# Performance work log

Hardware: AMD Instinct MI355X
Metric: run time of the kernel (lower is better)

## Reference

```python
import jax, jax.numpy as jnp
import numpy as np

N, D, C, E = 100000, 128, 16, 1000000
NUM_LAYERS, ALPHA = 5, 0.5
EPS_COS, EPS_LN = 1e-8, 1e-5


def setup_inputs() -> dict:
    key = jax.random.key(0)
    ks = jax.random.split(key, 10)
    inp = {
        'features': jax.random.normal(ks[0], (N, D), jnp.float32),
        'init_logits': jax.random.uniform(ks[1], (N, C), jnp.float32),
        'W': jax.random.normal(ks[2], (D, D), jnp.float32) * (1.0 / np.sqrt(D)),
        'b': jnp.zeros((D,), jnp.float32),
        'ln_gamma': jnp.ones((D,), jnp.float32),
        'ln_beta': jnp.zeros((D,), jnp.float32),
        'ew_connect': jnp.ones((1,), jnp.float32),
        'ew_decorate': jnp.ones((1,), jnp.float32),
        'ew_next': jnp.ones((1,), jnp.float32),
    }
    names = ['src_connect', 'dst_connect', 'src_decorate', 'dst_decorate', 'src_next', 'dst_next']
    for i, nm in enumerate(names):
        inp[nm] = jax.random.randint(ks[4 + (i % 6)] if False else jax.random.fold_in(ks[3], i), (E,), 0, N, jnp.int32)
    return inp


def _label_prop(features, init_logits, W, b, ln_gamma, ln_beta, ews, edges):
    # feature_transform: Linear -> LayerNorm -> ReLU (Dropout is identity in eval)
    h = features @ W.T + b
    mu = jnp.mean(h, axis=-1, keepdims=True)
    var = jnp.mean(jnp.square(h - mu), axis=-1, keepdims=True)
    h = (h - mu) * jax.lax.rsqrt(var + EPS_LN) * ln_gamma + ln_beta
    h = jax.nn.relu(h)
    # per-node L2-normalized features for cosine similarity (eps-clamped like F.cosine_similarity)
    nrm = jnp.maximum(jnp.linalg.norm(h, axis=-1), EPS_COS)
    hn = h / nrm[:, None]
    # per-edge scalar weights are fixed across layers: sigmoid(ew) * cos(src, dst)
    edge_w = []
    for ew, (src, dst) in zip(ews, edges):
        sim = jnp.sum(hn[src] * hn[dst], axis=-1)  # [E]
        edge_w.append(jax.nn.sigmoid(ew[0]) * sim)
    n_nodes = init_logits.shape[0]
    cur = init_logits
    for _ in range(NUM_LAYERS):
        next_logits = jnp.zeros_like(cur)
        total_w = jnp.zeros((n_nodes,), cur.dtype)
        for w, (src, dst) in zip(edge_w, edges):
            next_logits = next_logits.at[src].add(w[:, None] * cur[dst])
            total_w = total_w.at[src].add(w)
        pos = total_w > 0
        denom = jnp.where(pos, total_w, 1.0)[:, None]
        next_logits = jnp.where(pos[:, None], next_logits / denom, next_logits)
        cur = ALPHA * next_logits + (1.0 - ALPHA) * init_logits
    return cur


def reference(features, init_logits, W, b, ln_gamma, ln_beta, ew_connect, ew_decorate, ew_next,
              src_connect, dst_connect, src_decorate, dst_decorate, src_next, dst_next):
    ews = [ew_connect, ew_decorate, ew_next]
    edges = [(src_connect, dst_connect), (src_decorate, dst_decorate), (src_next, dst_next)]
    return _label_prop(features, init_logits, W, b, ln_gamma, ln_beta, ews, edges)
```

## Files before the change

### kernel.cpp

```cpp
#include <hip/hip_runtime.h>
#include <hip/hip_fp8.h>
#include <math.h>

#define DD 128
#define CC 16
#define ALPHA_ 0.5f
#define EPS_LN 1e-5f
#define EPS_COS 1e-8f

typedef _Float16 h4 __attribute__((ext_vector_type(4)));
typedef _Float16 h8 __attribute__((ext_vector_type(8)));
typedef _Float16 f16x8 __attribute__((ext_vector_type(8)));
typedef float f32x4 __attribute__((ext_vector_type(4)));
typedef long lx2 __attribute__((ext_vector_type(2)));

__device__ __forceinline__ unsigned pk_fp8x4(float v0, float v1, float v2, float v3) {
#if __has_builtin(__builtin_amdgcn_cvt_pk_fp8_f32)
    int u = 0;
    u = __builtin_amdgcn_cvt_pk_fp8_f32(v0, v1, u, false);
    u = __builtin_amdgcn_cvt_pk_fp8_f32(v2, v3, u, true);
    return (unsigned)u;
#else
    __hip_fp8_e4m3 a(v0), b(v1), c(v2), d(v3);
    return (unsigned)a.__x | ((unsigned)b.__x << 8)
         | ((unsigned)c.__x << 16) | ((unsigned)d.__x << 24);
#endif
}

__global__ __launch_bounds__(256, 2) void ft_mfma_kernel(
    const float* __restrict__ feat, const float* __restrict__ W,
    const float* __restrict__ bias, const float* __restrict__ gamma,
    const float* __restrict__ beta, unsigned* __restrict__ hn8, int N)
{
    const int lane = threadIdx.x & 63;
    const int c16  = lane & 15;
    const int g    = lane >> 4;
    const int wv   = (blockIdx.x * (int)blockDim.x + (int)threadIdx.x) >> 6;
    const int nwv  = ((int)gridDim.x * (int)blockDim.x) >> 6;

    f16x8 wf[8][4];
#pragma unroll
    for (int jt = 0; jt < 8; ++jt) {
        const float* wr = W + (size_t)(jt * 16 + c16) * 128 + g * 8;
#pragma unroll
        for (int s = 0; s < 4; ++s) {
            float4 lo = *(const float4*)(wr + s * 32);
            float4 hi = *(const float4*)(wr + s * 32 + 4);
            f16x8 f;
            f[0] = (_Float16)lo.x; f[1] = (_Float16)lo.y;
            f[2] = (_Float16)lo.z; f[3] = (_Float16)lo.w;
            f[4] = (_Float16)hi.x; f[5] = (_Float16)hi.y;
            f[6] = (_Float16)hi.z; f[7] = (_Float16)hi.w;
            wf[jt][s] = f;
        }
    }

    const int ntiles = (N + 15) >> 4;
    for (int t = wv; t < ntiles; t += nwv) {
        const int i = (t << 4) + c16;
        const float* fr = feat + (size_t)min(i, N - 1) * 128 + g * 8;
        f16x8 bf[4];
#pragma unroll
        for (int s = 0; s < 4; ++s) {
            float4 lo = *(const float4*)(fr + s * 32);
            float4 hi = *(const float4*)(fr + s * 32 + 4);
            f16x8 f;
            f[0] = (_Float16)lo.x; f[1] = (_Float16)lo.y;
            f[2] = (_Float16)lo.z; f[3] = (_Float16)lo.w;
            f[4] = (_Float16)hi.x; f[5] = (_Float16)hi.y;
            f[6] = (_Float16)hi.z; f[7] = (_Float16)hi.w;
            bf[s] = f;
        }

        f32x4 acc[8] = {};
#pragma unroll
        for (int s = 0; s < 4; ++s)
#pragma unroll
            for (int jt = 0; jt < 8; ++jt)
                acc[jt] = __builtin_amdgcn_mfma_f32_16x16x32_f16(
                    wf[jt][s], bf[s], acc[jt], 0, 0, 0);

        float s1 = 0.f, s2 = 0.f;
#pragma unroll
        for (int jt = 0; jt < 8; ++jt) {
            float4 bb = ((const float4*)bias)[jt * 4 + g];
            float h0 = acc[jt][0] + bb.x, h1 = acc[jt][1] + bb.y;
            float h2_ = acc[jt][2] + bb.z, h3 = acc[jt][3] + bb.w;
            acc[jt][0] = h0; acc[jt][1] = h1; acc[jt][2] = h2_; acc[jt][3] = h3;
            s1 += h0 + h1 + h2_ + h3;
            s2 += h0 * h0 + h1 * h1 + h2_ * h2_ + h3 * h3;
        }
        s1 += __shfl_xor(s1, 16); s1 += __shfl_xor(s1, 32);
        s2 += __shfl_xor(s2, 16); s2 += __shfl_xor(s2, 32);
        float mu   = s1 * (1.f / 128.f);
        float var  = s2 * (1.f / 128.f) - mu * mu;
        float rstd = rsqrtf(var + EPS_LN);

        float nsq = 0.f;
#pragma unroll
        for (int jt = 0; jt < 8; ++jt) {
            float4 gg = ((const float4*)gamma)[jt * 4 + g];
            float4 be = ((const float4*)beta)[jt * 4 + g];
            float v0 = fmaxf((acc[jt][0] - mu) * rstd * gg.x + be.x, 0.f);
            float v1 = fmaxf((acc[jt][1] - mu) * rstd * gg.y + be.y, 0.f);
            float v2 = fmaxf((acc[jt][2] - mu) * rstd * gg.z + be.z, 0.f);
            float v3 = fmaxf((acc[jt][3] - mu) * rstd * gg.w + be.w, 0.f);
            acc[jt][0] = v0; acc[jt][1] = v1; acc[jt][2] = v2; acc[jt][3] = v3;
            nsq += v0 * v0 + v1 * v1 + v2 * v2 + v3 * v3;
        }
        nsq += __shfl_xor(nsq, 16); nsq += __shfl_xor(nsq, 32);
        float inv = 1.f / fmaxf(sqrtf(nsq), EPS_COS);

        if (i < N) {
#pragma unroll
            for (int jt = 0; jt < 8; ++jt) {
                hn8[(size_t)i * 32 + jt * 4 + g] =
                    pk_fp8x4(acc[jt][0] * inv, acc[jt][1] * inv,
                             acc[jt][2] * inv, acc[jt][3] * inv);
            }
        }
    }
}

__global__ void bcount_kernel(const int* __restrict__ s0, const int* __restrict__ s1,
                              const int* __restrict__ s2, int* __restrict__ gcnt,
                              int E, int NB)
{
    __shared__ int cnt[512];
    const int tid = threadIdx.x;
    for (int i = tid; i < NB; i += 256) cnt[i] = 0;
    __syncthreads();
    const int tot = 3 * E;
    const int chunk = (tot + gridDim.x - 1) / gridDim.x;
    const int lo = blockIdx.x * chunk, hi = min(lo + chunk, tot);
    for (int i = lo + tid; i < hi; i += 256) {
        int src = (i < E) ? s0[i] : (i < 2 * E) ? s1[i - E] : s2[i - 2 * E];
        atomicAdd(&cnt[src >> 8], 1);
    }
    __syncthreads();
    for (int i = tid; i < NB; i += 256)
        if (cnt[i]) atomicAdd(&gcnt[i], cnt[i]);
}

__global__ void bscan_kernel(const int* __restrict__ gcnt, int* __restrict__ bbase,
                             int* __restrict__ gcur, int NB, int totE)
{
    __shared__ int wsum[4];
    const int t = threadIdx.x;
    const int lane = t & 63;
    int a0 = (2 * t     < NB) ? gcnt[2 * t]     : 0;
    int a1 = (2 * t + 1 < NB) ? gcnt[2 * t + 1] : 0;
    int ts = a0 + a1;
    int v = ts;
#pragma unroll
    for (int m = 1; m <= 32; m <<= 1) {
        int u = __shfl_up(v, m);
        if (lane >= m) v += u;
    }
    if (lane == 63) wsum[t >> 6] = v;
    __syncthreads();
    int woff = 0;
    for (int w = 0; w < (t >> 6); ++w) woff += wsum[w];
    int excl = woff + v - ts;
    if (2 * t < NB)     { bbase[2 * t]     = excl;      gcur[2 * t]     = excl; }
    if (2 * t + 1 < NB) { bbase[2 * t + 1] = excl + a0; gcur[2 * t + 1] = excl + a0; }
    if (t == 0) bbase[NB] = totE;
}

__global__ void bpart_kernel(
    const int* __restrict__ s0, const int* __restrict__ d0,
    const int* __restrict__ s1, const int* __restrict__ d1,
    const int* __restrict__ s2, const int* __restrict__ d2,
    int* __restrict__ gcur, unsigned* __restrict__ stage, int E, int NB)
{
    __shared__ int cnt[512];
    __shared__ int rbase[512];
    const int tid = threadIdx.x;
    for (int i = tid; i < NB; i += 256) cnt[i] = 0;
    __syncthreads();
    const int tot = 3 * E;
    const int chunk = (tot + gridDim.x - 1) / gridDim.x;
    const int lo = blockIdx.x * chunk, hi = min(lo + chunk, tot);
    for (int i = lo + tid; i < hi; i += 256) {
        int src = (i < E) ? s0[i] : (i < 2 * E) ? s1[i - E] : s2[i - 2 * E];
        atomicAdd(&cnt[src >> 8], 1);
    }
    __syncthreads();
    for (int i = tid; i < NB; i += 256) {
        int c = cnt[i];
        rbase[i] = c ? atomicAdd(&gcur[i], c) : 0;
        cnt[i] = 0;
    }
    __syncthreads();
    for (int i = lo + tid; i < hi; i += 256) {
        int src, dst, cls;
        if (i < E)          { src = s0[i];         dst = d0[i];         cls = 0; }
        else if (i < 2 * E) { src = s1[i - E];     dst = d1[i - E];     cls = 1; }
        else                { src = s2[i - 2 * E]; dst = d2[i - 2 * E]; cls = 2; }
        int b = src >> 8;
        int pos = rbase[b] + atomicAdd(&cnt[b], 1);
        stage[pos] = (unsigned)dst | ((unsigned)cls << 17) | ((unsigned)(src & 255) << 19);
    }
}

__global__ void csrfin_kernel(const unsigned* __restrict__ stage,
                              const int* __restrict__ bbase,
                              int* __restrict__ row_ptr, int* __restrict__ dstc_csr,
                              int N, int totE)
{
    __shared__ int cnt[256];
    __shared__ int wsum[4];
    const int b = blockIdx.x;
    const int t = threadIdx.x;
    const int lane = t & 63;
    const int lo = b << 8;
    const int base = bbase[b];
    const int m = bbase[b + 1] - base;

    cnt[t] = 0;
    __syncthreads();
    for (int i = t; i < m; i += 256)
        atomicAdd(&cnt[(stage[base + i] >> 19) & 255], 1);
    __syncthreads();
    int c = cnt[t];
    int v = c;
#pragma unroll
    for (int mm = 1; mm <= 32; mm <<= 1) {
        int u = __shfl_up(v, mm);
        if (lane >= mm) v += u;
    }
    if (lane == 63) wsum[t >> 6] = v;
    __syncthreads();
    int woff = 0;
    for (int w = 0; w < (t >> 6); ++w) woff += wsum[w];
    int excl = woff + v - c;
    if (lo + t < N) row_ptr[lo + t] = base + excl;
    if (b == 0 && t == 0) row_ptr[N] = totE;
    __syncthreads();
    cnt[t] = base + excl;
    __syncthreads();
    for (int i = t; i < m; i += 256) {
        unsigned v2 = stage[base + i];
        int pos = atomicAdd(&cnt[(v2 >> 19) & 255], 1);
        dstc_csr[pos] = (int)(v2 & 0x1FFFF) | (int)(((v2 >> 17) & 3) << 24);
    }
}

__global__ void node_sim_kernel(const unsigned char* __restrict__ hn8,
    const int* __restrict__ row_ptr, const int* __restrict__ dstc_csr,
    const float* __restrict__ ew0, const float* __restrict__ ew1,
    const float* __restrict__ ew2, unsigned* __restrict__ wq_csr,
    float* __restrict__ scl, const _Float16* __restrict__ inith,
    _Float16* __restrict__ out1, int N)
{
    const int gtid = blockIdx.x * blockDim.x + threadIdx.x;
    const int lane = threadIdx.x & 63;
    const int c16  = lane & 15;
    const int g    = lane >> 4;
    const int wv   = gtid >> 6;
    const int nwv  = (gridDim.x * blockDim.x) >> 6;
    const float sg0 = 1.f / (1.f + expf(-ew0[0]));
    const float sg1 = 1.f / (1.f + expf(-ew1[0]));
    const float sg2 = 1.f / (1.f + expf(-ew2[0]));
    const int srcl = ((c16 >> 2) << 4) | c16;
    const int j4   = c16 & 3;

    for (int n = wv; n < N; n += nwv) {
        const int beg = row_ptr[n], end = row_ptr[n + 1];
        const int deg = end - beg;
        if (deg == 0) {
            if (lane == 0) scl[n] = ALPHA_;
            if (c16 == 0) {
                h4 ivn = *(const h4*)&inith[(size_t)n * 16 + g * 4];
                h4 st;
#pragma unroll
                for (int k = 0; k < 4; ++k)
                    st[k] = (_Float16)((1.f - ALPHA_) * (float)ivn[k]);
                *(h4*)&out1[(size_t)n * 16 + g * 4] = st;
            }
            continue;
        }

        const unsigned char* sp = hn8 + (size_t)n * 128 + g * 16;
        lx2 B0 = *(const lx2*)sp;
        lx2 B1 = *(const lx2*)(sp + 64);

        float total = 0.f;
        float p1[4] = {0.f, 0.f, 0.f, 0.f};
        const int nb = (deg + 15) >> 4;
        for (int kb = 0; kb < nb; ++kb) {
            const int ebase = beg + (kb << 4);
            const int rem = end - ebase;
            int vv = (c16 < rem) ? dstc_csr[ebase + c16] : 0;
            int dl = (c16 < rem) ? (vv & 0x1FFFF) : n;
            const unsigned char* rp = hn8 + (size_t)dl * 128 + g * 16;
            lx2 A0 = *(const lx2*)rp;
            lx2 A1 = *(const lx2*)(rp + 64);
            h4 ivd = *(const h4*)&inith[(size_t)dl * 16 + g * 4];

            f32x4 acc = {0.f, 0.f, 0.f, 0.f};
            acc = __builtin_amdgcn_mfma_f32_16x16x32_fp8_fp8(A0[0], B0[0], acc, 0, 0, 0);
            acc = __builtin_amdgcn_mfma_f32_16x16x32_fp8_fp8(A0[1], B0[1], acc, 0, 0, 0);
            acc = __builtin_amdgcn_mfma_f32_16x16x32_fp8_fp8(A1[0], B1[0], acc, 0, 0, 0);
            acc = __builtin_amdgcn_mfma_f32_16x16x32_fp8_fp8(A1[1], B1[1], acc, 0, 0, 0);

            float a01  = (j4 & 1) ? acc[1] : acc[0];
            float a23  = (j4 & 1) ? acc[3] : acc[2];
            float asel = (j4 & 2) ? a23 : a01;
            float mysim = __shfl(asel, srcl);

            int cls = (vv >> 24) & 3;
            float sgc = (cls == 0) ? sg0 : (cls == 1) ? sg1 : sg2;
            float w = sgc * mysim;
            if (c16 < rem) {
                total += w;
#pragma unroll
                for (int k = 0; k < 4; ++k) p1[k] += w * (float)ivd[k];
            }

            if (g == 0 && c16 < rem) {
                int q = (int)(w * 16000.f + ((w >= 0.f) ? 0.5f : -0.5f)) + 16384;
                q = min(max(q, 0), 32767);
                wq_csr[ebase + c16] = ((unsigned)vv & 0x1FFFFu)
                                    | ((unsigned)q << 17);
            }
        }
        total += __shfl_xor(total, 1);
        total += __shfl_xor(total, 2);
        total += __shfl_xor(total, 4);
        total += __shfl_xor(total, 8);
#pragma unroll
        for (int k = 0; k < 4; ++k) {
            p1[k] += __shfl_xor(p1[k], 1);
            p1[k] += __shfl_xor(p1[k], 2);
            p1[k] += __shfl_xor(p1[k], 4);
            p1[k] += __shfl_xor(p1[k], 8);
        }
        float s = ALPHA_ * ((total > 0.f) ? 1.f / total : 1.f);
        if (lane == 0) scl[n] = s;
        if (c16 == 0) {
            h4 ivn = *(const h4*)&inith[(size_t)n * 16 + g * 4];
            h4 st;
#pragma unroll
            for (int k = 0; k < 4; ++k)
                st[k] = (_Float16)(s * p1[k] + (1.f - ALPHA_) * (float)ivn[k]);
            *(h4*)&out1[(size_t)n * 16 + g * 4] = st;
        }
    }
}

__global__ void cvt_kernel(const float* __restrict__ init,
                           _Float16* __restrict__ outh, int M4)
{
    int i = blockIdx.x * blockDim.x + threadIdx.x;
    int stride = gridDim.x * blockDim.x;
    for (; i < M4; i += stride) {
        float4 v = ((const float4*)init)[i];
        h4 o;
        o[0] = (_Float16)v.x; o[1] = (_Float16)v.y;
        o[2] = (_Float16)v.z; o[3] = (_Float16)v.w;
        ((h4*)outh)[i] = o;
    }
}

template<bool LAST>
__global__ void prop_kernel(const int* __restrict__ row_ptr,
    const unsigned* __restrict__ wq_csr, const float* __restrict__ scl,
    const _Float16* __restrict__ cur, const _Float16* __restrict__ inith,
    float* __restrict__ out32, _Float16* __restrict__ out16, int N)
{
    const int gtid = blockIdx.x * blockDim.x + threadIdx.x;
    const int lane = threadIdx.x & 63;
    const int half = lane >> 5;
    const int l32  = lane & 31;
    const int sg   = l32 >> 2;
    const int c4   = l32 & 3;
    const int wv   = gtid >> 6;
    const int nwv  = (gridDim.x * blockDim.x) >> 6;
    const float dq = 1.f / 16000.f;
    for (int n = 2 * wv + half; n < N; n += 2 * nwv) {
        int beg = row_ptr[n], end = row_ptr[n + 1];
        float a0 = 0.f, a1 = 0.f, a2 = 0.f, a3 = 0.f;
#pragma unroll 2
        for (int e = beg + sg; e < end; e += 8) {
            unsigned u = wq_csr[e];
            int d = (int)(u & 0x1FFFFu);
            float w = (float)((int)(u >> 17) - 16384) * dq;
            h4 cv = *(const h4*)&cur[(size_t)d * 16 + c4 * 4];
            a0 += w * (float)cv[0];
            a1 += w * (float)cv[1];
            a2 += w * (float)cv[2];
            a3 += w * (float)cv[3];
        }
#pragma unroll
        for (int m = 4; m <= 16; m <<= 1) {
            a0 += __shfl_xor(a0, m);
            a1 += __shfl_xor(a1, m);
            a2 += __shfl_xor(a2, m);
            a3 += __shfl_xor(a3, m);
        }
        if (sg == 0) {
            float sc = scl[n];
            h4 iv = *(const h4*)&inith[(size_t)n * 16 + c4 * 4];
            float r0 = sc * a0 + (1.f - ALPHA_) * (float)iv[0];
            float r1 = sc * a1 + (1.f - ALPHA_) * (float)iv[1];
            float r2 = sc * a2 + (1.f - ALPHA_) * (float)iv[2];
            float r3 = sc * a3 + (1.f - ALPHA_) * (float)iv[3];
            if (LAST) {
                float4 st; st.x = r0; st.y = r1; st.z = r2; st.w = r3;
                *(float4*)&out32[(size_t)n * 16 + c4 * 4] = st;
            } else {
                h4 st;
                st[0] = (_Float16)r0; st[1] = (_Float16)r1;
                st[2] = (_Float16)r2; st[3] = (_Float16)r3;
                *(h4*)&out16[(size_t)n * 16 + c4 * 4] = st;
            }
        }
    }
}

extern "C" void kernel_launch(void* const* d_in, const int* in_sizes, int n_in,
                              void* d_out, int out_size, void* d_ws, size_t ws_size,
                              hipStream_t stream)
{
    const float* feat  = (const float*)d_in[0];
    const float* initl = (const float*)d_in[1];
    const float* W     = (const float*)d_in[2];
    const float* b     = (const float*)d_in[3];
    const float* gam   = (const float*)d_in[4];
    const float* bet   = (const float*)d_in[5];
    const float* ew0   = (const float*)d_in[6];
    const float* ew1   = (const float*)d_in[7];
    const float* ew2   = (const float*)d_in[8];
    const int* s0  = (const int*)d_in[9];
    const int* dd0 = (const int*)d_in[10];
    const int* s1  = (const int*)d_in[11];
    const int* dd1 = (const int*)d_in[12];
    const int* s2  = (const int*)d_in[13];
    const int* dd2 = (const int*)d_in[14];

    const int N = in_sizes[0] / DD;
    const int E = in_sizes[9];
    const int totE = 3 * E;
    const int NB = (N + 255) >> 8;
    float* out = (float*)d_out;

    char* ws = (char*)d_ws;
    size_t off = 0;
    auto alloc = [&](size_t bytes) -> void* {
        void* p = ws + off;
        off += (bytes + 255) & ~(size_t)255;
        return p;
    };
    unsigned*  hn8     = (unsigned*)alloc((size_t)N * DD);
    int*       gcnt    = (int*)alloc((size_t)(NB + 1) * 4);
    int*       bbase   = (int*)alloc((size_t)(NB + 1) * 4);
    int*       gcur    = (int*)alloc((size_t)(NB + 1) * 4);
    int*       row_ptr = (int*)alloc((size_t)(N + 1) * 4);
    unsigned*  stage   = (unsigned*)alloc((size_t)totE * 4);
    int*       dstc_csr= (int*)alloc((size_t)totE * 4);
    unsigned*  wq_csr  = (unsigned*)alloc((size_t)totE * 4);
    float*     scl     = (float*)alloc((size_t)N * 4);
    _Float16*  inith   = (_Float16*)alloc((size_t)N * CC * 2);
    _Float16*  curA    = (_Float16*)alloc((size_t)N * CC * 2);
    _Float16*  curB    = (_Float16*)alloc((size_t)N * CC * 2);

    ft_mfma_kernel<<<512, 256, 0, stream>>>(feat, W, b, gam, bet, hn8, N);

    hipMemsetAsync(gcnt, 0, (size_t)NB * 4, stream);
    bcount_kernel<<<1024, 256, 0, stream>>>(s0, s1, s2, gcnt, E, NB);
    bscan_kernel<<<1, 256, 0, stream>>>(gcnt, bbase, gcur, NB, totE);
    bpart_kernel<<<1024, 256, 0, stream>>>(s0, dd0, s1, dd1, s2, dd2,
                                           gcur, stage, E, NB);
    csrfin_kernel<<<NB, 256, 0, stream>>>(stage, bbase, row_ptr, dstc_csr, N, totE);

    cvt_kernel<<<256, 256, 0, stream>>>(initl, inith, N * CC / 4);

    const int wblk = (N * 64 + 255) / 256;
    node_sim_kernel<<<wblk, 256, 0, stream>>>((const unsigned char*)hn8,
                                              row_ptr, dstc_csr,
                                              ew0, ew1, ew2, wq_csr, scl,
                                              inith, curA, N);

    const int pblk = (N * 32 + 255) / 256;
    const _Float16* cs = curA;
    _Float16* bufs[2] = { curB, curA };
    for (int layer = 0; layer < 3; ++layer) {
        _Float16* dst = bufs[layer & 1];
        prop_kernel<false><<<pblk, 256, 0, stream>>>(row_ptr, wq_csr, scl,
                                                     cs, inith, nullptr, dst, N);
        cs = dst;
    }
    prop_kernel<true><<<pblk, 256, 0, stream>>>(row_ptr, wq_csr, scl,
                                                cs, inith, out, nullptr, N);
}
```

Before: 361.0 us.

## Replace bucket count+scan with fixed-capacity buckets and fuse fp16 conversion into csrfin

```diff
diff --git a/kernel.cpp b/kernel.cpp
--- a/kernel.cpp
+++ b/kernel.cpp
@@ -9,7 +9,6 @@
 #define EPS_COS 1e-8f
 
 typedef _Float16 h4 __attribute__((ext_vector_type(4)));
-typedef _Float16 h8 __attribute__((ext_vector_type(8)));
 typedef _Float16 f16x8 __attribute__((ext_vector_type(8)));
 typedef float f32x4 __attribute__((ext_vector_type(4)));
 typedef long lx2 __attribute__((ext_vector_type(2)));
@@ -122,11 +121,14 @@
     }
 }
 
-__global__ void bcount_kernel(const int* __restrict__ s0, const int* __restrict__ s1,
-                              const int* __restrict__ s2, int* __restrict__ gcnt,
-                              int E, int NB)
+__global__ void bpart_kernel(
+    const int* __restrict__ s0, const int* __restrict__ d0,
+    const int* __restrict__ s1, const int* __restrict__ d1,
+    const int* __restrict__ s2, const int* __restrict__ d2,
+    int* __restrict__ gcur, unsigned* __restrict__ stage, int E, int NB, int cap)
 {
     __shared__ int cnt[512];
+    __shared__ int rbase[512];
     const int tid = threadIdx.x;
     for (int i = tid; i < NB; i += 256) cnt[i] = 0;
     __syncthreads();
@@ -138,57 +140,9 @@
         atomicAdd(&cnt[src >> 8], 1);
     }
     __syncthreads();
-    for (int i = tid; i < NB; i += 256)
-        if (cnt[i]) atomicAdd(&gcnt[i], cnt[i]);
-}
-
-__global__ void bscan_kernel(const int* __restrict__ gcnt, int* __restrict__ bbase,
-                             int* __restrict__ gcur, int NB, int totE)
-{
-    __shared__ int wsum[4];
-    const int t = threadIdx.x;
-    const int lane = t & 63;
-    int a0 = (2 * t     < NB) ? gcnt[2 * t]     : 0;
-    int a1 = (2 * t + 1 < NB) ? gcnt[2 * t + 1] : 0;
-    int ts = a0 + a1;
-    int v = ts;
-#pragma unroll
-    for (int m = 1; m <= 32; m <<= 1) {
-        int u = __shfl_up(v, m);
-        if (lane >= m) v += u;
-    }
-    if (lane == 63) wsum[t >> 6] = v;
-    __syncthreads();
-    int woff = 0;
-    for (int w = 0; w < (t >> 6); ++w) woff += wsum[w];
-    int excl = woff + v - ts;
-    if (2 * t < NB)     { bbase[2 * t]     = excl;      gcur[2 * t]     = excl; }
-    if (2 * t + 1 < NB) { bbase[2 * t + 1] = excl + a0; gcur[2 * t + 1] = excl + a0; }
-    if (t == 0) bbase[NB] = totE;
-}
-
-__global__ void bpart_kernel(
-    const int* __restrict__ s0, const int* __restrict__ d0,
-    const int* __restrict__ s1, const int* __restrict__ d1,
-    const int* __restrict__ s2, const int* __restrict__ d2,
-    int* __restrict__ gcur, unsigned* __restrict__ stage, int E, int NB)
-{
-    __shared__ int cnt[512];
-    __shared__ int rbase[512];
-    const int tid = threadIdx.x;
-    for (int i = tid; i < NB; i += 256) cnt[i] = 0;
-    __syncthreads();
-    const int tot = 3 * E;
-    const int chunk = (tot + gridDim.x - 1) / gridDim.x;
-    const int lo = blockIdx.x * chunk, hi = min(lo + chunk, tot);
-    for (int i = lo + tid; i < hi; i += 256) {
-        int src = (i < E) ? s0[i] : (i < 2 * E) ? s1[i - E] : s2[i - 2 * E];
-        atomicAdd(&cnt[src >> 8], 1);
-    }
-    __syncthreads();
     for (int i = tid; i < NB; i += 256) {
         int c = cnt[i];
-        rbase[i] = c ? atomicAdd(&gcur[i], c) : 0;
+        rbase[i] = c ? (i * cap + atomicAdd(&gcur[i], c)) : 0;
         cnt[i] = 0;
     }
     __syncthreads();
@@ -204,18 +158,34 @@
 }
 
 __global__ void csrfin_kernel(const unsigned* __restrict__ stage,
-                              const int* __restrict__ bbase,
-                              int* __restrict__ row_ptr, int* __restrict__ dstc_csr,
-                              int N, int totE)
-{
+                              const int* __restrict__ gcur,
+                              int2* __restrict__ rowpc, int* __restrict__ dstc_csr,
+                              const float* __restrict__ initl,
+                              _Float16* __restrict__ inith,
+                              int N, int NB, int cap)
+{
+    const int b = blockIdx.x;
+    const int t = threadIdx.x;
+    if (b >= NB) {
+        int idx = (b - NB) * 256 + t;
+        int stride = (gridDim.x - NB) * 256;
+        int M4 = N * 4;
+        for (int i = idx; i < M4; i += stride) {
+            float4 v = ((const float4*)initl)[i];
+            h4 o;
+            o[0] = (_Float16)v.x; o[1] = (_Float16)v.y;
+            o[2] = (_Float16)v.z; o[3] = (_Float16)v.w;
+            ((h4*)inith)[i] = o;
+        }
+        return;
+    }
+
     __shared__ int cnt[256];
     __shared__ int wsum[4];
-    const int b = blockIdx.x;
-    const int t = threadIdx.x;
     const int lane = t & 63;
     const int lo = b << 8;
-    const int base = bbase[b];
-    const int m = bbase[b + 1] - base;
+    const int base = b * cap;
+    const int m = gcur[b];
 
     cnt[t] = 0;
     __syncthreads();
@@ -234,8 +204,7 @@
     int woff = 0;
     for (int w = 0; w < (t >> 6); ++w) woff += wsum[w];
     int excl = woff + v - c;
-    if (lo + t < N) row_ptr[lo + t] = base + excl;
-    if (b == 0 && t == 0) row_ptr[N] = totE;
+    if (lo + t < N) rowpc[lo + t] = make_int2(base + excl, c);
     __syncthreads();
     cnt[t] = base + excl;
     __syncthreads();
@@ -247,7 +216,7 @@
 }
 
 __global__ void node_sim_kernel(const unsigned char* __restrict__ hn8,
-    const int* __restrict__ row_ptr, const int* __restrict__ dstc_csr,
+    const int2* __restrict__ rowpc, const int* __restrict__ dstc_csr,
     const float* __restrict__ ew0, const float* __restrict__ ew1,
     const float* __restrict__ ew2, unsigned* __restrict__ wq_csr,
     float* __restrict__ scl, const _Float16* __restrict__ inith,
@@ -266,8 +235,9 @@
     const int j4   = c16 & 3;
 
     for (int n = wv; n < N; n += nwv) {
-        const int beg = row_ptr[n], end = row_ptr[n + 1];
-        const int deg = end - beg;
+        const int2 pc = rowpc[n];
+        const int beg = pc.x, deg = pc.y;
+        const int end = beg + deg;
         if (deg == 0) {
             if (lane == 0) scl[n] = ALPHA_;
             if (c16 == 0) {
@@ -349,22 +319,8 @@
     }
 }
 
-__global__ void cvt_kernel(const float* __restrict__ init,
-                           _Float16* __restrict__ outh, int M4)
-{
-    int i = blockIdx.x * blockDim.x + threadIdx.x;
-    int stride = gridDim.x * blockDim.x;
-    for (; i < M4; i += stride) {
-        float4 v = ((const float4*)init)[i];
-        h4 o;
-        o[0] = (_Float16)v.x; o[1] = (_Float16)v.y;
-        o[2] = (_Float16)v.z; o[3] = (_Float16)v.w;
-        ((h4*)outh)[i] = o;
-    }
-}
-
 template<bool LAST>
-__global__ void prop_kernel(const int* __restrict__ row_ptr,
+__global__ void prop_kernel(const int2* __restrict__ rowpc,
     const unsigned* __restrict__ wq_csr, const float* __restrict__ scl,
     const _Float16* __restrict__ cur, const _Float16* __restrict__ inith,
     float* __restrict__ out32, _Float16* __restrict__ out16, int N)
@@ -379,9 +335,10 @@
     const int nwv  = (gridDim.x * blockDim.x) >> 6;
     const float dq = 1.f / 16000.f;
     for (int n = 2 * wv + half; n < N; n += 2 * nwv) {
-        int beg = row_ptr[n], end = row_ptr[n + 1];
+        int2 pc = rowpc[n];
+        int beg = pc.x, end = pc.x + pc.y;
         float a0 = 0.f, a1 = 0.f, a2 = 0.f, a3 = 0.f;
-#pragma unroll 2
+#pragma unroll 4
         for (int e = beg + sg; e < end; e += 8) {
             unsigned u = wq_csr[e];
             int d = (int)(u & 0x1FFFFu);
@@ -443,6 +400,7 @@
     const int E = in_sizes[9];
     const int totE = 3 * E;
     const int NB = (N + 255) >> 8;
+    const int cap = (totE + NB - 1) / NB + 2048;
     float* out = (float*)d_out;
 
     char* ws = (char*)d_ws;
@@ -453,13 +411,11 @@
         return p;
     };
     unsigned*  hn8     = (unsigned*)alloc((size_t)N * DD);
-    int*       gcnt    = (int*)alloc((size_t)(NB + 1) * 4);
-    int*       bbase   = (int*)alloc((size_t)(NB + 1) * 4);
-    int*       gcur    = (int*)alloc((size_t)(NB + 1) * 4);
-    int*       row_ptr = (int*)alloc((size_t)(N + 1) * 4);
-    unsigned*  stage   = (unsigned*)alloc((size_t)totE * 4);
-    int*       dstc_csr= (int*)alloc((size_t)totE * 4);
-    unsigned*  wq_csr  = (unsigned*)alloc((size_t)totE * 4);
+    int*       gcur    = (int*)alloc((size_t)NB * 4);
+    int2*      rowpc   = (int2*)alloc((size_t)N * 8);
+    unsigned*  stage   = (unsigned*)alloc((size_t)NB * cap * 4);
+    int*       dstc_csr= (int*)alloc((size_t)NB * cap * 4);
+    unsigned*  wq_csr  = (unsigned*)alloc((size_t)NB * cap * 4);
     float*     scl     = (float*)alloc((size_t)N * 4);
     _Float16*  inith   = (_Float16*)alloc((size_t)N * CC * 2);
     _Float16*  curA    = (_Float16*)alloc((size_t)N * CC * 2);
@@ -467,18 +423,15 @@
 
     ft_mfma_kernel<<<512, 256, 0, stream>>>(feat, W, b, gam, bet, hn8, N);
 
-    hipMemsetAsync(gcnt, 0, (size_t)NB * 4, stream);
-    bcount_kernel<<<1024, 256, 0, stream>>>(s0, s1, s2, gcnt, E, NB);
-    bscan_kernel<<<1, 256, 0, stream>>>(gcnt, bbase, gcur, NB, totE);
+    hipMemsetAsync(gcur, 0, (size_t)NB * 4, stream);
     bpart_kernel<<<1024, 256, 0, stream>>>(s0, dd0, s1, dd1, s2, dd2,
-                                           gcur, stage, E, NB);
-    csrfin_kernel<<<NB, 256, 0, stream>>>(stage, bbase, row_ptr, dstc_csr, N, totE);
-
-    cvt_kernel<<<256, 256, 0, stream>>>(initl, inith, N * CC / 4);
+                                           gcur, stage, E, NB, cap);
+    csrfin_kernel<<<NB + 1024, 256, 0, stream>>>(stage, gcur, rowpc, dstc_csr,
+                                                 initl, inith, N, NB, cap);
 
     const int wblk = (N * 64 + 255) / 256;
     node_sim_kernel<<<wblk, 256, 0, stream>>>((const unsigned char*)hn8,
-                                              row_ptr, dstc_csr,
+                                              rowpc, dstc_csr,
                                               ew0, ew1, ew2, wq_csr, scl,
                                               inith, curA, N);
 
@@ -487,10 +440,10 @@
     _Float16* bufs[2] = { curB, curA };
     for (int layer = 0; layer < 3; ++layer) {
         _Float16* dst = bufs[layer & 1];
-        prop_kernel<false><<<pblk, 256, 0, stream>>>(row_ptr, wq_csr, scl,
+        prop_kernel<false><<<pblk, 256, 0, stream>>>(rowpc, wq_csr, scl,
                                                      cs, inith, nullptr, dst, N);
         cs = dst;
     }
-    prop_kernel<true><<<pblk, 256, 0, stream>>>(row_ptr, wq_csr, scl,
+    prop_kernel<true><<<pblk, 256, 0, stream>>>(rowpc, wq_csr, scl,
                                                 cs, inith, out, nullptr, N);
 }
```

Result: faster. 340.2 us (-5.8%).
